# Kernel optimization log

Measured on AMD Instinct MI355X. Metric: run time of the kernel, lower is better.

The kernel has to match this reference:

```python
import jax, jax.numpy as jnp
import numpy as np

B, N, H, F, K = 64, 64, 256, 8, 2
E = N * (N - 1)


def _lin(k, fan_in, fan_out):
    return jax.random.normal(k, (fan_in, fan_out), jnp.float32) / np.sqrt(fan_in)


def setup_inputs() -> dict:
    key = jax.random.key(0)
    ks = jax.random.split(key, 20)
    # fully-connected directed edge list (no self loops), as in __init__
    idx = np.array([[i, j] for i in range(N) for j in range(N) if i != j], dtype=np.int64).T
    inp = {
        "inputs": jax.random.normal(ks[0], (B, N, F), jnp.float32),
        "hidden": jax.random.normal(ks[1], (B, N, H), jnp.float32),
        "edges": jax.random.uniform(ks[2], (E, K), jnp.float32),
        "edge_index": jnp.asarray(idx),
        # EdgeDecoder MLP: Linear(2H,2H) -> ELU -> Linear(2H,H)
        "ed_w1": _lin(ks[3], 2 * H, 2 * H), "ed_b1": jnp.full((2 * H,), 0.1, jnp.float32),
        "ed_w2": _lin(ks[4], 2 * H, H), "ed_b2": jnp.full((H,), 0.1, jnp.float32),
        # GRU-style hidden linears (no bias)
        "wr": _lin(ks[5], H, H), "wi": _lin(ks[6], H, H), "wh": _lin(ks[7], H, H),
        # input linears (with bias)
        "ir_w": _lin(ks[8], F, H), "ir_b": jnp.full((H,), 0.1, jnp.float32),
        "ii_w": _lin(ks[9], F, H), "ii_b": jnp.full((H,), 0.1, jnp.float32),
        "in_w": _lin(ks[10], F, H), "in_b": jnp.full((H,), 0.1, jnp.float32),
        # output MLP
        "f1_w": _lin(ks[11], H, H), "f1_b": jnp.full((H,), 0.1, jnp.float32),
        "f2_w": _lin(ks[12], H, H), "f2_b": jnp.full((H,), 0.1, jnp.float32),
        "f3_w": _lin(ks[13], H, F), "f3_b": jnp.full((F,), 0.1, jnp.float32),
    }
    return inp


def reference(inputs, hidden, edges, edge_index,
              ed_w1, ed_b1, ed_w2, ed_b2,
              wr, wi, wh,
              ir_w, ir_b, ii_w, ii_b, in_w, in_b,
              f1_w, f1_b, f2_w, f2_b, f3_w, f3_b):
    # convert_edge_index: max over edge-type dim -> per-edge scalar weight [E]
    w = jnp.max(edges, axis=-1)
    src, dst = edge_index[0], edge_index[1]   # PyG: x_j = x[src], x_i = x[dst]
    x_j = hidden[:, src]                      # [B,E,H] gather (irregular)
    x_i = hidden[:, dst]                      # [B,E,H]
    ef = jnp.concatenate([x_i, x_j], axis=-1) * w[None, :, None]   # [B,E,2H]
    # EdgeDecoder.mlp (dropout inactive in eval)
    m = jax.nn.elu(ef @ ed_w1 + ed_b1) @ ed_w2 + ed_b2             # [B,E,H]
    # mean-aggregate messages at receiver nodes (each node has N-1 in-edges)
    agg = jax.ops.segment_sum(m.transpose(1, 0, 2), dst, num_segments=N)
    agg = agg.transpose(1, 0, 2) / (N - 1)                         # [B,N,H]
    # GRU-style update
    r = jax.nn.sigmoid(inputs @ ir_w + ir_b + agg @ wr)
    i = jax.nn.sigmoid(inputs @ ii_w + ii_b + agg @ wi)
    n = jnp.tanh(inputs @ in_w + in_b + r * (agg @ wh))
    new_hidden = (1.0 - i) * n + i * hidden
    # output MLP with residual on inputs (dropout inactive in eval)
    pred = jax.nn.relu(new_hidden @ f1_w + f1_b)
    pred = jax.nn.relu(pred @ f2_w + f2_b)
    pred = inputs + (pred @ f3_w + f3_b)
    return pred, new_hidden
```

## Files before the change

### kernel.cpp

```cpp
#include <hip/hip_runtime.h>
#include <hip/hip_bf16.h>
#include <math.h>

#define BB 64
#define NN 64
#define HH 256
#define FF 8

typedef __bf16 bf16;
typedef bf16 bf16x2 __attribute__((ext_vector_type(2)));
typedef bf16 bf16x4 __attribute__((ext_vector_type(4)));
typedef bf16 bf16x8 __attribute__((ext_vector_type(8)));
typedef float f32x2 __attribute__((ext_vector_type(2)));
typedef float f32x4 __attribute__((ext_vector_type(4)));

#define GLL(g, l) __builtin_amdgcn_global_load_lds( \
    (const __attribute__((address_space(1))) void*)(g), \
    (__attribute__((address_space(3))) void*)(l), 16, 0, 0)

#define MFMA(a, b, c) __builtin_amdgcn_mfma_f32_16x16x32_bf16(a, b, c, 0, 0, 0)

#define WAITVM2 do { asm volatile("s_waitcnt vmcnt(2)" ::: "memory"); \
                     __builtin_amdgcn_sched_barrier(0); } while (0)
#define WAITVM0 do { asm volatile("s_waitcnt vmcnt(0)" ::: "memory"); \
                     __builtin_amdgcn_sched_barrier(0); } while (0)
#define SBAR __builtin_amdgcn_sched_barrier(0)

__device__ __forceinline__ f32x2 unpk(unsigned int u) {
    union { unsigned int i; float f; } a, b;
    a.i = (u & 0xffffu) << 16;
    b.i = u & 0xffff0000u;
    f32x2 r; r.x = a.f; r.y = b.f; return r;
}

__device__ __forceinline__ bf16x8 frag128(const char* base, int row, int cbyte) {
    const int sw = (row & 7) << 4;
    const int a = row * 128 + cbyte;
    bf16x4 lo = *(const bf16x4*)(base + (a ^ sw));
    bf16x4 hi = *(const bf16x4*)(base + ((a + 32) ^ sw));
    return __builtin_shufflevector(lo, hi, 0, 1, 2, 3, 4, 5, 6, 7);
}

__device__ __forceinline__ bf16x8 frag512(const char* base, int row, int cbyte) {
    const int sw = (row & 7) << 4;
    const int a = row * 512 + cbyte;
    bf16x4 lo = *(const bf16x4*)(base + (a ^ sw));
    bf16x4 hi = *(const bf16x4*)(base + ((a + 32) ^ sw));
    return __builtin_shufflevector(lo, hi, 0, 1, 2, 3, 4, 5, 6, 7);
}

__device__ __forceinline__ bf16x8 frag1024(const char* base, int row, int cbyte) {
    const int sw = (row & 7) << 4;
    const int a = row * 1024 + cbyte;
    bf16x4 lo = *(const bf16x4*)(base + (a ^ sw));
    bf16x4 hi = *(const bf16x4*)(base + ((a + 32) ^ sw));
    return __builtin_shufflevector(lo, hi, 0, 1, 2, 3, 4, 5, 6, 7);
}

__device__ __forceinline__ void st512(char* base, int row, int col, bf16 v) {
    *(bf16*)(base + ((row * 512 + col * 2) ^ ((row & 7) << 4))) = v;
}

__global__ __launch_bounds__(256) void g1pack_kernel(
    const float* __restrict__ hidden, const float* __restrict__ ed_w1,
    const float* __restrict__ ed_w2,
    const float* __restrict__ wr, const float* __restrict__ wi,
    const float* __restrict__ wh,
    const float* __restrict__ f1_w, const float* __restrict__ f2_w,
    bf16* __restrict__ PQ, bf16* __restrict__ W2t, bf16* __restrict__ Wg,
    bf16* __restrict__ f1t, bf16* __restrict__ f2t)
{
    __shared__ __align__(1024) char smem[49408];
    const int tid = threadIdx.x;

    if (blockIdx.y >= 64) {
        const int t = (blockIdx.y - 64) * 16 + blockIdx.x;
        const float* src; bf16* dst; int R, C, tile;
        if (t < 32) { src = ed_w2; dst = W2t; R = 512; C = 256; tile = t; }
        else {
            int m = (t - 32) >> 4; tile = (t - 32) & 15; R = 256; C = 256;
            const float* ss[5] = {wr, wi, wh, f1_w, f2_w};
            bf16* dd[5] = {Wg, Wg + 65536, Wg + 131072, f1t, f2t};
            src = ss[m]; dst = dd[m];
        }
        const int tc = C >> 6;
        const int k0 = (tile / tc) * 64, n0 = (tile % tc) * 64;
        float (*ls)[65] = (float(*)[65])smem;
        {
            int rr = tid >> 2, cc = (tid & 3) * 16;
            const float* sp = src + (size_t)(k0 + rr) * C + n0 + cc;
#pragma unroll
            for (int j = 0; j < 16; j += 4) {
                float4 v = *(const float4*)(sp + j);
                ls[rr][cc + j] = v.x; ls[rr][cc + j + 1] = v.y;
                ls[rr][cc + j + 2] = v.z; ls[rr][cc + j + 3] = v.w;
            }
        }
        __syncthreads();
        {
            int n = tid >> 2, kc = (tid & 3) * 16;
            bf16x8 o0, o1;
#pragma unroll
            for (int j = 0; j < 8; ++j) o0[j] = (bf16)ls[kc + j][n];
#pragma unroll
            for (int j = 0; j < 8; ++j) o1[j] = (bf16)ls[kc + 8 + j][n];
            bf16* dp = dst + (size_t)(n0 + n) * R + k0 + kc;
            *(bf16x8*)dp = o0;
            *(bf16x8*)(dp + 8) = o1;
        }
        return;
    }

    char* Bs = smem;
    char* pool = smem + 32768;
    const int wave = tid >> 6, lane = tid & 63;
    const int wr_ = wave >> 1, wc_ = wave & 1;
    const int l15 = lane & 15, l4 = lane >> 4;
    const int bm = blockIdx.y * 64, bn = blockIdx.x * 64;
    const int roff = (bn >= 512) ? 256 : 0;
    const int ncol = bn & 511;

    {
        float (*ls)[65] = (float(*)[65])pool;
#pragma unroll
        for (int kt = 0; kt < 4; ++kt) {
            {
                int rr = tid >> 2, cc = (tid & 3) * 16;
                const float* sp = ed_w1 + (size_t)(kt * 64 + roff + rr) * 512 + ncol + cc;
#pragma unroll
                for (int j = 0; j < 16; j += 4) {
                    float4 v = *(const float4*)(sp + j);
                    ls[rr][cc + j] = v.x; ls[rr][cc + j + 1] = v.y;
                    ls[rr][cc + j + 2] = v.z; ls[rr][cc + j + 3] = v.w;
                }
            }
            __syncthreads();
            {
                int n = tid >> 2, kc = (tid & 3) * 16;
                bf16x8 o0, o1;
#pragma unroll
                for (int j = 0; j < 8; ++j) o0[j] = (bf16)ls[kc + j][n];
#pragma unroll
                for (int j = 0; j < 8; ++j) o1[j] = (bf16)ls[kc + 8 + j][n];
                int cb0 = kt * 8 + (kc >> 3);
                char* rowp = Bs + n * 512;
                *(bf16x8*)(rowp + ((cb0 ^ (n & 7)) * 16)) = o0;
                *(bf16x8*)(rowp + (((cb0 + 1) ^ (n & 7)) * 16)) = o1;
            }
            __syncthreads();
        }
    }

    f32x4 acc[2][2];
#pragma unroll
    for (int mf = 0; mf < 2; ++mf)
#pragma unroll
        for (int nf = 0; nf < 2; ++nf)
            acc[mf][nf] = (f32x4){0.f, 0.f, 0.f, 0.f};

    auto stageA = [&](int buf, int kt) {
        char* Ab = pool + buf * 8192;
#pragma unroll
        for (int a = 0; a < 2; ++a) {
            int idx = a * 256 + tid;
            int row = idx >> 3, cb = idx & 7;
            const float* gp = hidden + (size_t)(bm + row) * 256 + kt * 64 + cb * 8;
            float4 v0 = *(const float4*)gp;
            float4 v1 = *(const float4*)(gp + 4);
            bf16x8 o;
            o[0] = (bf16)v0.x; o[1] = (bf16)v0.y; o[2] = (bf16)v0.z; o[3] = (bf16)v0.w;
            o[4] = (bf16)v1.x; o[5] = (bf16)v1.y; o[6] = (bf16)v1.z; o[7] = (bf16)v1.w;
            *(bf16x8*)(Ab + row * 128 + ((cb ^ (row & 7)) * 16)) = o;
        }
    };

    auto computeT = [&](int buf, int kt) {
        char* Ab = pool + buf * 8192;
#pragma unroll
        for (int kk = 0; kk < 2; ++kk) {
            bf16x8 af[2];
#pragma unroll
            for (int mf = 0; mf < 2; ++mf)
                af[mf] = frag128(Ab, wr_ * 32 + mf * 16 + l15, kk * 64 + l4 * 8);
#pragma unroll
            for (int nf = 0; nf < 2; ++nf) {
                bf16x8 bfr = frag512(Bs, wc_ * 32 + nf * 16 + l15,
                                     kt * 128 + kk * 64 + l4 * 8);
#pragma unroll
                for (int mf = 0; mf < 2; ++mf)
                    acc[mf][nf] = MFMA(af[mf], bfr, acc[mf][nf]);
            }
        }
    };

    stageA(0, 0);
    __syncthreads();
#pragma unroll
    for (int t = 0; t < 4; ++t) {
        if (t < 3) stageA((t + 1) & 1, t + 1);
        computeT(t & 1, t);
        __syncthreads();
    }

#pragma unroll
    for (int mf = 0; mf < 2; ++mf)
#pragma unroll
        for (int nf = 0; nf < 2; ++nf)
#pragma unroll
            for (int r = 0; r < 4; ++r) {
                int grow = bm + wr_ * 32 + mf * 16 + l4 * 4 + r;
                int col = bn + wc_ * 32 + nf * 16 + l15;
                PQ[(size_t)grow * 1024 + col] = (bf16)acc[mf][nf][r];
            }
}

__global__ __launch_bounds__(1024) void fused_kernel(
    const bf16* __restrict__ PQ, const float* __restrict__ edges,
    const float* __restrict__ b1,
    const bf16* __restrict__ W2t, const float* __restrict__ ed_b2,
    const bf16* __restrict__ Wg,
    const bf16* __restrict__ f1t, const float* __restrict__ f1_b,
    const bf16* __restrict__ f2t, const float* __restrict__ f2_b,
    const float* __restrict__ f3_w, const float* __restrict__ f3_b,
    const float* __restrict__ inputs, const float* __restrict__ hidden,
    const float* __restrict__ irw, const float* __restrict__ irb,
    const float* __restrict__ iiw, const float* __restrict__ iib,
    const float* __restrict__ inw, const float* __restrict__ inb,
    float* __restrict__ NH, float* __restrict__ pred)
{
    __shared__ __align__(1024) char smem[102400];
    char* qs   = smem;
    char* sl   = smem + 65536;
    float* f3s = (float*)(smem + 65536);
    char* h1l  = smem + 73728;
    char* aggl = smem + 81920;
    char* h2l  = smem + 81920;
    char* nhl  = smem + 90112;
    float (*wls)[16] = (float(*)[16])(smem + 98304);

    const int tid = threadIdx.x;
    const int wave = tid >> 6, lane = tid & 63;
    const int l15 = lane & 15, l4 = lane >> 4;
    const int srow = lane >> 3;
    const int scol = ((lane & 7) ^ (lane >> 3)) * 8;
    const int vb = (blockIdx.x & 7) * 32 + (blockIdx.x >> 3);
    const int b = vb >> 2, d0 = (vb & 3) * 16;
    const bf16* Pb = PQ + (size_t)(b * 64) * 1024;
    char* mybuf = qs + wave * 4096;
    const int n0 = wave * 16;

    auto stageB = [&](const bf16* Wt, int Krow, int bufi, int kt) {
        char* d = mybuf + bufi * 2048;
#pragma unroll
        for (int s = 0; s < 2; ++s)
            GLL(Wt + (size_t)(n0 + s * 8 + srow) * Krow + kt * 64 + scol,
                d + s * 1024 + lane * 16);
    };

#pragma unroll
    for (int si = 0; si < 4; ++si) {
        int row = wave * 4 + si;
        GLL(Pb + (size_t)row * 1024 + 512 + lane * 8, qs + row * 1024 + lane * 16);
    }
    {
        int src = tid >> 4, dc = tid & 15, d = d0 + dc;
        float w = 0.f;
        if (src != d) {
            int e = src * 63 + (d < src ? d : d - 1);
            float2 ev = ((const float2*)edges)[e];
            w = fmaxf(ev.x, ev.y);
        }
        wls[src][dc] = w;
    }
    const int c = tid & 255, hh = tid >> 8;
    f32x2 p2[4];
#pragma unroll
    for (int dd = 0; dd < 4; ++dd)
        p2[dd] = unpk(*(const unsigned int*)(Pb + (size_t)(d0 + hh * 4 + dd) * 1024 + 2 * c));
    float2 bbl = *(const float2*)(b1 + 2 * c);
    f32x2 bb; bb.x = bbl.x; bb.y = bbl.y;
    __syncthreads();

    {
        f32x2 acc[4];
#pragma unroll
        for (int dd = 0; dd < 4; ++dd) acc[dd] = (f32x2){0.f, 0.f};
        const unsigned int* Qs32 = (const unsigned int*)qs;
#pragma unroll 4
        for (int src = 0; src < 64; ++src) {
            f32x2 qv = unpk(Qs32[src * 256 + c]);
            float4 wv = *(const float4*)&wls[src][hh * 4];
            float w[4] = {wv.x, wv.y, wv.z, wv.w};
#pragma unroll
            for (int dd = 0; dd < 4; ++dd) {
                f32x2 w2v; w2v.x = w[dd]; w2v.y = w[dd];
                f32x2 v = (p2[dd] + qv) * w2v + bb;
                float e0 = __expf(v.x) - 1.f;
                float e1 = __expf(v.y) - 1.f;
                f32x2 r;
                r.x = (v.x > 0.f) ? v.x : e0;
                r.y = (v.y > 0.f) ? v.y : e1;
                acc[dd] += r;
            }
        }
        f32x2 selfc;
        selfc.x = (bb.x > 0.f) ? bb.x : (__expf(bb.x) - 1.f);
        selfc.y = (bb.y > 0.f) ? bb.y : (__expf(bb.y) - 1.f);
#pragma unroll
        for (int dd = 0; dd < 4; ++dd) {
            int row = hh * 4 + dd;
            bf16x2 st;
            st[0] = (bf16)(acc[dd].x - selfc.x);
            st[1] = (bf16)(acc[dd].y - selfc.y);
            *(bf16x2*)(sl + ((row * 1024 + 4 * c) ^ ((row & 7) << 4))) = st;
        }
    }
    __syncthreads();

    {
        f32x4 a1 = (f32x4){0.f, 0.f, 0.f, 0.f};
        stageB(W2t, 512, 0, 0);
#pragma unroll
        for (int kt = 0; kt < 8; ++kt) {
            if (kt < 7) { SBAR; stageB(W2t, 512, (kt + 1) & 1, kt + 1); WAITVM2; }
            else { SBAR; WAITVM0; }
            const char* bbuf = mybuf + (kt & 1) * 2048;
#pragma unroll
            for (int kk = 0; kk < 2; ++kk) {
                bf16x8 af = frag1024(sl, l15, kt * 128 + kk * 64 + l4 * 8);
                a1 = MFMA(af, frag128(bbuf, l15, kk * 64 + l4 * 8), a1);
            }
        }
        int col = n0 + l15;
        float eb = ed_b2[col];
#pragma unroll
        for (int r = 0; r < 4; ++r)
            st512(aggl, l4 * 4 + r, col, (bf16)(a1[r] * (1.f / 63.f) + eb));
    }
    __syncthreads();

    for (int i = tid; i < 2048; i += 1024) f3s[i] = f3_w[i];

    {
        f32x4 a2[3];
#pragma unroll
        for (int g = 0; g < 3; ++g) a2[g] = (f32x4){0.f, 0.f, 0.f, 0.f};
        stageB(Wg, 256, 0, 0);
#pragma unroll
        for (int st_ = 0; st_ < 12; ++st_) {
            const int g = st_ >> 2, kt = st_ & 3;
            if (st_ < 11) {
                const int nx = st_ + 1;
                SBAR;
                stageB(Wg + (size_t)(nx >> 2) * 65536, 256, nx & 1, nx & 3);
                WAITVM2;
            } else { SBAR; WAITVM0; }
            const char* bbuf = mybuf + (st_ & 1) * 2048;
#pragma unroll
            for (int kk = 0; kk < 2; ++kk) {
                bf16x8 af = frag512(aggl, l15, kt * 128 + kk * 64 + l4 * 8);
                a2[g] = MFMA(af, frag128(bbuf, l15, kk * 64 + l4 * 8), a2[g]);
            }
        }
        const int col = n0 + l15;
        float w8r[8], w8i[8], w8n[8];
#pragma unroll
        for (int f = 0; f < 8; ++f) {
            w8r[f] = irw[f * 256 + col];
            w8i[f] = iiw[f * 256 + col];
            w8n[f] = inw[f * 256 + col];
        }
        const float xr0 = irb[col], xi0 = iib[col], xn0 = inb[col];
#pragma unroll
        for (int r = 0; r < 4; ++r) {
            const int lrow = l4 * 4 + r;
            const int grow = b * 64 + d0 + lrow;
            const float* inp = inputs + (size_t)grow * 8;
            float xr = xr0, xi = xi0, xn = xn0;
#pragma unroll
            for (int f = 0; f < 8; ++f) {
                float x = inp[f];
                xr += x * w8r[f]; xi += x * w8i[f]; xn += x * w8n[f];
            }
            float aR = a2[0][r];
            float aI = a2[1][r];
            float aN = a2[2][r];
            float rg = __builtin_amdgcn_rcpf(1.f + __expf(-(xr + aR)));
            float ig = __builtin_amdgcn_rcpf(1.f + __expf(-(xi + aI)));
            float tz = xn + rg * aN;
            tz = fminf(fmaxf(tz, -15.f), 15.f);
            float e2x = __expf(2.f * tz);
            float nn = (e2x - 1.f) * __builtin_amdgcn_rcpf(e2x + 1.f);
            size_t o = (size_t)grow * 256 + col;
            float nh = (1.f - ig) * nn + ig * hidden[o];
            NH[o] = nh;
            st512(nhl, lrow, col, (bf16)nh);
        }
    }
    __syncthreads();

    {
        f32x4 a1 = (f32x4){0.f, 0.f, 0.f, 0.f};
        stageB(f1t, 256, 0, 0);
#pragma unroll
        for (int kt = 0; kt < 4; ++kt) {
            if (kt < 3) { SBAR; stageB(f1t, 256, (kt + 1) & 1, kt + 1); WAITVM2; }
            else { SBAR; WAITVM0; }
            const char* bbuf = mybuf + (kt & 1) * 2048;
#pragma unroll
            for (int kk = 0; kk < 2; ++kk) {
                bf16x8 af = frag512(nhl, l15, kt * 128 + kk * 64 + l4 * 8);
                a1 = MFMA(af, frag128(bbuf, l15, kk * 64 + l4 * 8), a1);
            }
        }
        int col = n0 + l15;
        float bv = f1_b[col];
#pragma unroll
        for (int r = 0; r < 4; ++r)
            st512(h1l, l4 * 4 + r, col, (bf16)fmaxf(a1[r] + bv, 0.f));
    }
    __syncthreads();

    {
        f32x4 a1 = (f32x4){0.f, 0.f, 0.f, 0.f};
        stageB(f2t, 256, 0, 0);
#pragma unroll
        for (int kt = 0; kt < 4; ++kt) {
            if (kt < 3) { SBAR; stageB(f2t, 256, (kt + 1) & 1, kt + 1); WAITVM2; }
            else { SBAR; WAITVM0; }
            const char* bbuf = mybuf + (kt & 1) * 2048;
#pragma unroll
            for (int kk = 0; kk < 2; ++kk) {
                bf16x8 af = frag512(h1l, l15, kt * 128 + kk * 64 + l4 * 8);
                a1 = MFMA(af, frag128(bbuf, l15, kk * 64 + l4 * 8), a1);
            }
        }
        int col = n0 + l15;
        float bv = f2_b[col];
#pragma unroll
        for (int r = 0; r < 4; ++r)
            st512(h2l, l4 * 4 + r, col, (bf16)fmaxf(a1[r] + bv, 0.f));
    }
    __syncthreads();

    if (tid < 128) {
        const int row = tid >> 3, f = tid & 7;
        const int sw = (row & 7) << 4;
        float a = f3_b[f];
        for (int k0 = 0; k0 < 256; k0 += 8) {
            bf16x8 h8 = *(const bf16x8*)(h2l + ((row * 512 + k0 * 2) ^ sw));
#pragma unroll
            for (int j = 0; j < 8; ++j)
                a += (float)h8[j] * f3s[(k0 + j) * 8 + f];
        }
        int gi = (b * 64 + d0 + row) * 8 + f;
        pred[gi] = inputs[gi] + a;
    }
}

extern "C" void kernel_launch(void* const* d_in, const int* in_sizes, int n_in,
                              void* d_out, int out_size, void* d_ws, size_t ws_size,
                              hipStream_t stream) {
    const float* inputs = (const float*)d_in[0];
    const float* hidden = (const float*)d_in[1];
    const float* edges  = (const float*)d_in[2];
    const float* ed_w1 = (const float*)d_in[4];
    const float* ed_b1 = (const float*)d_in[5];
    const float* ed_w2 = (const float*)d_in[6];
    const float* ed_b2 = (const float*)d_in[7];
    const float* wr = (const float*)d_in[8];
    const float* wi = (const float*)d_in[9];
    const float* wh = (const float*)d_in[10];
    const float* ir_w = (const float*)d_in[11];
    const float* ir_b = (const float*)d_in[12];
    const float* ii_w = (const float*)d_in[13];
    const float* ii_b = (const float*)d_in[14];
    const float* in_w = (const float*)d_in[15];
    const float* in_b = (const float*)d_in[16];
    const float* f1_w = (const float*)d_in[17];
    const float* f1_b = (const float*)d_in[18];
    const float* f2_w = (const float*)d_in[19];
    const float* f2_b = (const float*)d_in[20];
    const float* f3_w = (const float*)d_in[21];
    const float* f3_b = (const float*)d_in[22];

    float* out = (float*)d_out;
    float* pred = out;
    float* NH = out + (size_t)BB * NN * FF;

    bf16* bws = (bf16*)d_ws;
    bf16* PQ   = bws;
    bf16* W2t  = bws + 4194304;
    bf16* Wg   = bws + 4325376;
    bf16* f1t  = bws + 4521984;
    bf16* f2t  = bws + 4587520;

    g1pack_kernel<<<dim3(16, 71), dim3(256), 0, stream>>>(
        hidden, ed_w1, ed_w2, wr, wi, wh, f1_w, f2_w,
        PQ, W2t, Wg, f1t, f2t);

    fused_kernel<<<dim3(256), dim3(1024), 0, stream>>>(
        PQ, edges, ed_b1, W2t, ed_b2, Wg, f1t, f1_b, f2t, f2_b,
        f3_w, f3_b, inputs, hidden,
        ir_w, ir_b, ii_w, ii_b, in_w, in_b, NH, pred);
}
```

Before: 66.35 us.

## Shrink fused kernel LDS footprint by halving Q staging and single-buffering weights

Cuts the fused kernel's shared memory from 100KB to 80KB so that two 1024-thread blocks can fit per CU. Q rows are now staged in two halves of 32 sources, with extra barriers between them. The weight tiles for the four MFMA stages drop from double to single buffering, with a full vmcnt(0) wait after each load. The intent is higher occupancy so other blocks hide latency, at the cost of serializing each weight load with its compute inside a block and adding synchronisation.

After: 73.63 us. +11.0%, slower.

```diff
diff --git a/kernel.cpp b/kernel.cpp
--- a/kernel.cpp
+++ b/kernel.cpp
@@ -20,8 +20,6 @@
 
 #define MFMA(a, b, c) __builtin_amdgcn_mfma_f32_16x16x32_bf16(a, b, c, 0, 0, 0)
 
-#define WAITVM2 do { asm volatile("s_waitcnt vmcnt(2)" ::: "memory"); \
-                     __builtin_amdgcn_sched_barrier(0); } while (0)
 #define WAITVM0 do { asm volatile("s_waitcnt vmcnt(0)" ::: "memory"); \
                      __builtin_amdgcn_sched_barrier(0); } while (0)
 #define SBAR __builtin_amdgcn_sched_barrier(0)
@@ -214,7 +212,7 @@
             }
 }
 
-__global__ __launch_bounds__(1024) void fused_kernel(
+__global__ __launch_bounds__(1024, 8) void fused_kernel(
     const bf16* __restrict__ PQ, const float* __restrict__ edges,
     const float* __restrict__ b1,
     const bf16* __restrict__ W2t, const float* __restrict__ ed_b2,
@@ -228,15 +226,16 @@
     const float* __restrict__ inw, const float* __restrict__ inb,
     float* __restrict__ NH, float* __restrict__ pred)
 {
-    __shared__ __align__(1024) char smem[102400];
+    __shared__ __align__(1024) char smem[81920];
     char* qs   = smem;
+    char* aggl = smem;
+    char* nhl  = smem + 8192;
+    float* f3s = (float*)(smem + 16384);
+    char* h1l  = smem + 24576;
+    float (*wls)[16] = (float(*)[16])(smem + 32768);
+    char* bbase = smem + 32768;
     char* sl   = smem + 65536;
-    float* f3s = (float*)(smem + 65536);
-    char* h1l  = smem + 73728;
-    char* aggl = smem + 81920;
-    char* h2l  = smem + 81920;
-    char* nhl  = smem + 90112;
-    float (*wls)[16] = (float(*)[16])(smem + 98304);
+    char* h2l  = smem + 65536;
 
     const int tid = threadIdx.x;
     const int wave = tid >> 6, lane = tid & 63;
@@ -246,20 +245,19 @@
     const int vb = (blockIdx.x & 7) * 32 + (blockIdx.x >> 3);
     const int b = vb >> 2, d0 = (vb & 3) * 16;
     const bf16* Pb = PQ + (size_t)(b * 64) * 1024;
-    char* mybuf = qs + wave * 4096;
+    char* mybuf = bbase + wave * 2048;
     const int n0 = wave * 16;
 
-    auto stageB = [&](const bf16* Wt, int Krow, int bufi, int kt) {
-        char* d = mybuf + bufi * 2048;
+    auto stageB = [&](const bf16* Wt, int Krow, int kt) {
 #pragma unroll
         for (int s = 0; s < 2; ++s)
             GLL(Wt + (size_t)(n0 + s * 8 + srow) * Krow + kt * 64 + scol,
-                d + s * 1024 + lane * 16);
+                mybuf + s * 1024 + lane * 16);
     };
 
 #pragma unroll
-    for (int si = 0; si < 4; ++si) {
-        int row = wave * 4 + si;
+    for (int si = 0; si < 2; ++si) {
+        int row = wave * 2 + si;
         GLL(Pb + (size_t)row * 1024 + 512 + lane * 8, qs + row * 1024 + lane * 16);
     }
     {
@@ -281,13 +279,13 @@
     f32x2 bb; bb.x = bbl.x; bb.y = bbl.y;
     __syncthreads();
 
-    {
-        f32x2 acc[4];
-#pragma unroll
-        for (int dd = 0; dd < 4; ++dd) acc[dd] = (f32x2){0.f, 0.f};
-        const unsigned int* Qs32 = (const unsigned int*)qs;
+    f32x2 acc[4];
+#pragma unroll
+    for (int dd = 0; dd < 4; ++dd) acc[dd] = (f32x2){0.f, 0.f};
+    const unsigned int* Qs32 = (const unsigned int*)qs;
+    {
 #pragma unroll 4
-        for (int src = 0; src < 64; ++src) {
+        for (int src = 0; src < 32; ++src) {
             f32x2 qv = unpk(Qs32[src * 256 + c]);
             float4 wv = *(const float4*)&wls[src][hh * 4];
             float w[4] = {wv.x, wv.y, wv.z, wv.w};
@@ -303,6 +301,33 @@
                 acc[dd] += r;
             }
         }
+    }
+    __syncthreads();
+#pragma unroll
+    for (int si = 0; si < 2; ++si) {
+        int row = wave * 2 + si;
+        GLL(Pb + (size_t)(32 + row) * 1024 + 512 + lane * 8,
+            qs + row * 1024 + lane * 16);
+    }
+    __syncthreads();
+    {
+#pragma unroll 4
+        for (int src = 32; src < 64; ++src) {
+            f32x2 qv = unpk(Qs32[(src - 32) * 256 + c]);
+            float4 wv = *(const float4*)&wls[src][hh * 4];
+            float w[4] = {wv.x, wv.y, wv.z, wv.w};
+#pragma unroll
+            for (int dd = 0; dd < 4; ++dd) {
+                f32x2 w2v; w2v.x = w[dd]; w2v.y = w[dd];
+                f32x2 v = (p2[dd] + qv) * w2v + bb;
+                float e0 = __expf(v.x) - 1.f;
+                float e1 = __expf(v.y) - 1.f;
+                f32x2 r;
+                r.x = (v.x > 0.f) ? v.x : e0;
+                r.y = (v.y > 0.f) ? v.y : e1;
+                acc[dd] += r;
+            }
+        }
         f32x2 selfc;
         selfc.x = (bb.x > 0.f) ? bb.x : (__expf(bb.x) - 1.f);
         selfc.y = (bb.y > 0.f) ? bb.y : (__expf(bb.y) - 1.f);
@@ -319,16 +344,13 @@
 
     {
         f32x4 a1 = (f32x4){0.f, 0.f, 0.f, 0.f};
-        stageB(W2t, 512, 0, 0);
 #pragma unroll
         for (int kt = 0; kt < 8; ++kt) {
-            if (kt < 7) { SBAR; stageB(W2t, 512, (kt + 1) & 1, kt + 1); WAITVM2; }
-            else { SBAR; WAITVM0; }
-            const char* bbuf = mybuf + (kt & 1) * 2048;
+            SBAR; stageB(W2t, 512, kt); WAITVM0;
 #pragma unroll
             for (int kk = 0; kk < 2; ++kk) {
                 bf16x8 af = frag1024(sl, l15, kt * 128 + kk * 64 + l4 * 8);
-                a1 = MFMA(af, frag128(bbuf, l15, kk * 64 + l4 * 8), a1);
+                a1 = MFMA(af, frag128(mybuf, l15, kk * 64 + l4 * 8), a1);
             }
         }
         int col = n0 + l15;
@@ -345,21 +367,14 @@
         f32x4 a2[3];
 #pragma unroll
         for (int g = 0; g < 3; ++g) a2[g] = (f32x4){0.f, 0.f, 0.f, 0.f};
-        stageB(Wg, 256, 0, 0);
 #pragma unroll
         for (int st_ = 0; st_ < 12; ++st_) {
             const int g = st_ >> 2, kt = st_ & 3;
-            if (st_ < 11) {
-                const int nx = st_ + 1;
-                SBAR;
-                stageB(Wg + (size_t)(nx >> 2) * 65536, 256, nx & 1, nx & 3);
-                WAITVM2;
-            } else { SBAR; WAITVM0; }
-            const char* bbuf = mybuf + (st_ & 1) * 2048;
+            SBAR; stageB(Wg + (size_t)g * 65536, 256, kt); WAITVM0;
 #pragma unroll
             for (int kk = 0; kk < 2; ++kk) {
                 bf16x8 af = frag512(aggl, l15, kt * 128 + kk * 64 + l4 * 8);
-                a2[g] = MFMA(af, frag128(bbuf, l15, kk * 64 + l4 * 8), a2[g]);
+                a2[g] = MFMA(af, frag128(mybuf, l15, kk * 64 + l4 * 8), a2[g]);
             }
         }
         const int col = n0 + l15;
@@ -401,16 +416,13 @@
 
     {
         f32x4 a1 = (f32x4){0.f, 0.f, 0.f, 0.f};
-        stageB(f1t, 256, 0, 0);
 #pragma unroll
         for (int kt = 0; kt < 4; ++kt) {
-            if (kt < 3) { SBAR; stageB(f1t, 256, (kt + 1) & 1, kt + 1); WAITVM2; }
-            else { SBAR; WAITVM0; }
-            const char* bbuf = mybuf + (kt & 1) * 2048;
+            SBAR; stageB(f1t, 256, kt); WAITVM0;
 #pragma unroll
             for (int kk = 0; kk < 2; ++kk) {
                 bf16x8 af = frag512(nhl, l15, kt * 128 + kk * 64 + l4 * 8);
-                a1 = MFMA(af, frag128(bbuf, l15, kk * 64 + l4 * 8), a1);
+                a1 = MFMA(af, frag128(mybuf, l15, kk * 64 + l4 * 8), a1);
             }
         }
         int col = n0 + l15;
@@ -423,16 +435,13 @@
 
     {
         f32x4 a1 = (f32x4){0.f, 0.f, 0.f, 0.f};
-        stageB(f2t, 256, 0, 0);
 #pragma unroll
         for (int kt = 0; kt < 4; ++kt) {
-            if (kt < 3) { SBAR; stageB(f2t, 256, (kt + 1) & 1, kt + 1); WAITVM2; }
-            else { SBAR; WAITVM0; }
-            const char* bbuf = mybuf + (kt & 1) * 2048;
+            SBAR; stageB(f2t, 256, kt); WAITVM0;
 #pragma unroll
             for (int kk = 0; kk < 2; ++kk) {
                 bf16x8 af = frag512(h1l, l15, kt * 128 + kk * 64 + l4 * 8);
-                a1 = MFMA(af, frag128(bbuf, l15, kk * 64 + l4 * 8), a1);
+                a1 = MFMA(af, frag128(mybuf, l15, kk * 64 + l4 * 8), a1);
             }
         }
         int col = n0 + l15;
```
